# Optimization experiments

Measured on AMD Instinct MI355X. Metric: run time of the kernel, lower is better.

## Reference

```python
import jax, jax.numpy as jnp
import numpy as np

DMODEL = 1024
DK = 64
DHEAD = 16
DEPTH = DK * DHEAD
N, LQ, L = 2, 2048, 2048


def setup_inputs() -> dict:
    key = jax.random.key(0)
    ks = jax.random.split(key, 12)
    s = 1.0 / np.sqrt(DMODEL)
    inp = {
        'x': jax.random.normal(ks[0], (N, LQ, DMODEL), jnp.float32),
        'y': jax.random.normal(ks[1], (N, L, DMODEL), jnp.float32),
        'mask': jnp.tril(jnp.ones((LQ, L), dtype=bool)),  # causal
        'Wq': jax.random.normal(ks[2], (DMODEL, DEPTH), jnp.float32) * s,
        'bq': jnp.zeros((DEPTH,), jnp.float32),
        'Wk': jax.random.normal(ks[3], (DMODEL, DEPTH), jnp.float32) * s,
        'bk': jnp.zeros((DEPTH,), jnp.float32),
        'Wv': jax.random.normal(ks[4], (DMODEL, DEPTH), jnp.float32) * s,
        'bv': jnp.zeros((DEPTH,), jnp.float32),
        'Wo': jax.random.normal(ks[5], (DEPTH, DMODEL), jnp.float32) * (1.0 / np.sqrt(DEPTH)),
        'bo': jnp.zeros((DMODEL,), jnp.float32),
    }
    return inp


def reference(x, y, mask, Wq, bq, Wk, bk, Wv, bv, Wo, bo):
    fac = 1.0 / np.sqrt(DK)
    q = (x @ Wq + bq).reshape(N, LQ, DHEAD, DK).transpose(0, 2, 1, 3)  # N,H,Lq,dk
    k = (y @ Wk + bk).reshape(N, L, DHEAD, DK).transpose(0, 2, 1, 3)   # N,H,L,dk
    v = (y @ Wv + bv).reshape(N, L, DHEAD, DK).transpose(0, 2, 1, 3)   # N,H,L,dk
    scores = jnp.einsum('bhqd,bhkd->bhqk', q, k) * fac                 # N,H,Lq,L
    scores = jnp.where(mask, scores, -1e9)  # mask broadcasts over N,H
    attn = jax.nn.softmax(scores, axis=-1)
    out = jnp.einsum('bhqk,bhkd->bhqd', attn, v)                        # N,H,Lq,dk
    out = out.transpose(0, 2, 1, 3).reshape(N, LQ, DEPTH)
    return out @ Wo + bo
```

## Files before the change

kernel.cpp:

```cpp
#include <hip/hip_runtime.h>
#include <hip/hip_bf16.h>

typedef __attribute__((ext_vector_type(8))) short short8;
typedef __attribute__((ext_vector_type(4))) float floatx4;

#define LQ 2048
#define DM 1024
#define NH 16
#define LOG2E 1.44269504088896f

typedef __attribute__((address_space(1))) void gas_t;
typedef __attribute__((address_space(3))) void las_t;

__device__ __forceinline__ void async16(const __hip_bfloat16* g, __hip_bfloat16* l) {
    __builtin_amdgcn_global_load_lds((gas_t*)g, (las_t*)l, 16, 0, 0);
}

__global__ __launch_bounds__(256) void prep_all(
    const float* __restrict__ x,  const float* __restrict__ y,
    const float* __restrict__ Wq, const float* __restrict__ Wk,
    const float* __restrict__ Wv, const float* __restrict__ Wo,
    __hip_bfloat16* __restrict__ xb,  __hip_bfloat16* __restrict__ yb,
    __hip_bfloat16* __restrict__ Wqt, __hip_bfloat16* __restrict__ Wkt,
    __hip_bfloat16* __restrict__ Wvt, __hip_bfloat16* __restrict__ Wot)
{
    __shared__ float tile[64][65];
    const int t  = threadIdx.x;
    const int bx = blockIdx.x;

    if (bx < 4096) {
        const float* in = (bx < 2048) ? x : y;
        __hip_bfloat16* out = (bx < 2048) ? xb : yb;
        const int i = ((bx & 2047) * 256 + t) * 8;
        float4 a0 = ((const float4*)(in + i))[0];
        float4 a1 = ((const float4*)(in + i))[1];
        union { __hip_bfloat16 h[8]; uint4 u; } pk;
        pk.h[0] = __float2bfloat16(a0.x); pk.h[1] = __float2bfloat16(a0.y);
        pk.h[2] = __float2bfloat16(a0.z); pk.h[3] = __float2bfloat16(a0.w);
        pk.h[4] = __float2bfloat16(a1.x); pk.h[5] = __float2bfloat16(a1.y);
        pk.h[6] = __float2bfloat16(a1.z); pk.h[7] = __float2bfloat16(a1.w);
        *(uint4*)(out + i) = pk.u;
        return;
    }

    const int r    = bx - 4096;
    const int wsel = r >> 8;
    const int tid  = r & 255;
    const int n0   = (tid & 15) * 64, k0 = (tid >> 4) * 64;
    const float* W = (wsel == 0) ? Wq : (wsel == 1) ? Wk : (wsel == 2) ? Wv : Wo;
    __hip_bfloat16* Wt = (wsel == 0) ? Wqt : (wsel == 1) ? Wkt : (wsel == 2) ? Wvt : Wot;

    const int rr0 = t >> 4, c4 = (t & 15) * 4;
#pragma unroll
    for (int rr = 0; rr < 64; rr += 16) {
        float4 v = *(const float4*)&W[(size_t)(k0 + rr0 + rr) * DM + n0 + c4];
        tile[rr0 + rr][c4 + 0] = v.x; tile[rr0 + rr][c4 + 1] = v.y;
        tile[rr0 + rr][c4 + 2] = v.z; tile[rr0 + rr][c4 + 3] = v.w;
    }
    __syncthreads();
    const int nr = t >> 2, kc = (t & 3) * 16;
    union { __hip_bfloat16 h[16]; uint4 u[2]; } pk;
#pragma unroll
    for (int i = 0; i < 16; ++i) pk.h[i] = __float2bfloat16(tile[kc + i][nr]);
    uint4* dst = (uint4*)&Wt[(size_t)(n0 + nr) * DM + k0 + kc];
    dst[0] = pk.u[0];
    dst[1] = pk.u[1];
}

__global__ __launch_bounds__(512) void gemm_qkv(
    const __hip_bfloat16* __restrict__ xb,
    const __hip_bfloat16* __restrict__ yb,
    const __hip_bfloat16* __restrict__ Bt,
    const float* __restrict__ bq, const float* __restrict__ bk,
    const float* __restrict__ bv,
    __hip_bfloat16* __restrict__ Qb, __hip_bfloat16* __restrict__ Kb,
    __hip_bfloat16* __restrict__ Vt,
    float qscl)
{
    constexpr int BM = 256, BN = 256, Kd = 1024;
    constexpr int NHS = Kd / 32;
    __shared__ __align__(16) __hip_bfloat16 As[4][256 * 32];
    __shared__ __align__(16) __hip_bfloat16 Bs[4][256 * 32];

    const int t    = threadIdx.x;
    const int w    = t >> 6;
    const int lane = t & 63;
    const int quad = lane >> 4;
    const int l16  = lane & 15;
    const int wm   = w & 1;
    const int wn   = w >> 1;

    const int f  = blockIdx.x;
    const int rx = f & 7;
    const int rr = f >> 3;
    const int bx = (rx & 1) * 6 + rr % 6;
    const int by = (rx >> 1) * 4 + rr / 6;
    const int m0 = by * BM;
    const int n0 = bx * BN;

    const int region = n0 >> 10;
    const int nl     = n0 & 1023;

    const __hip_bfloat16* A = (region == 0) ? xb : yb;

    floatx4 acc[8][4];
#pragma unroll
    for (int i = 0; i < 8; ++i)
#pragma unroll
        for (int j = 0; j < 4; ++j) acc[i][j] = (floatx4){0.f, 0.f, 0.f, 0.f};

    auto stageA = [&](int h) {
        const int k0 = h * 32, slot = h & 3;
#pragma unroll
        for (int l = 0; l < 2; ++l) {
            const int c   = l * 512 + t;
            const int row = c >> 2;
            const int ch  = (c & 3) ^ ((row >> 1) & 3);
            async16(A + (size_t)(m0 + row) * Kd + k0 + ch * 8, &As[slot][c * 8]);
        }
    };
    auto stageB = [&](int h) {
        const int k0 = h * 32, slot = h & 3;
#pragma unroll
        for (int l = 0; l < 2; ++l) {
            const int c   = l * 512 + t;
            const int row = c >> 2;
            const int ch  = (c & 3) ^ ((row >> 1) & 3);
            async16(Bt + (size_t)(n0 + row) * Kd + k0 + ch * 8, &Bs[slot][c * 8]);
        }
    };

    stageA(0); stageB(0); stageA(1); stageB(1);
    asm volatile("s_waitcnt vmcnt(4)" ::: "memory");
    __builtin_amdgcn_sched_barrier(0);
    __builtin_amdgcn_s_barrier();

    const int csw = (l16 >> 1) & 3;

    for (int h = 0; h < NHS; ++h) {
        const int slot = h & 3;
        const __hip_bfloat16* as = &As[slot][0];
        const __hip_bfloat16* bs = &Bs[slot][0];
        short8 af[8], bf[4];

#pragma unroll
        for (int nj = 0; nj < 4; ++nj) {
            const int row = wn * 64 + nj * 16 + l16;
            bf[nj] = *(const short8*)&bs[row * 32 + (quad ^ csw) * 8];
        }
#pragma unroll
        for (int mi = 0; mi < 4; ++mi) {
            const int row = wm * 128 + mi * 16 + l16;
            af[mi] = *(const short8*)&as[row * 32 + (quad ^ csw) * 8];
        }
        if (h + 2 < NHS) stageA(h + 2);
        __builtin_amdgcn_s_barrier();
        asm volatile("s_waitcnt lgkmcnt(0)" ::: "memory");
        __builtin_amdgcn_sched_barrier(0);
        __builtin_amdgcn_s_setprio(1);
#pragma unroll
        for (int mi = 0; mi < 4; ++mi)
#pragma unroll
            for (int nj = 0; nj < 4; ++nj)
                acc[mi][nj] = __builtin_amdgcn_mfma_f32_16x16x32_bf16(af[mi], bf[nj], acc[mi][nj], 0, 0, 0);
        __builtin_amdgcn_s_setprio(0);
        __builtin_amdgcn_s_barrier();

#pragma unroll
        for (int mi = 4; mi < 8; ++mi) {
            const int row = wm * 128 + mi * 16 + l16;
            af[mi] = *(const short8*)&as[row * 32 + (quad ^ csw) * 8];
        }
        if (h + 2 < NHS) stageB(h + 2);
        __builtin_amdgcn_s_barrier();
        asm volatile("s_waitcnt lgkmcnt(0)" ::: "memory");
        __builtin_amdgcn_sched_barrier(0);
        __builtin_amdgcn_s_setprio(1);
#pragma unroll
        for (int mi = 4; mi < 8; ++mi)
#pragma unroll
            for (int nj = 0; nj < 4; ++nj)
                acc[mi][nj] = __builtin_amdgcn_mfma_f32_16x16x32_bf16(af[mi], bf[nj], acc[mi][nj], 0, 0, 0);
        __builtin_amdgcn_s_setprio(0);
        if (h + 2 < NHS)      asm volatile("s_waitcnt vmcnt(4)" ::: "memory");
        else                  asm volatile("s_waitcnt vmcnt(0)" ::: "memory");
        __builtin_amdgcn_sched_barrier(0);
        __builtin_amdgcn_s_barrier();
    }

    if (region < 2) {
        __hip_bfloat16* C    = (region == 0) ? Qb : Kb;
        const float*    bias = (region == 0) ? bq : bk;
        const float     scl  = (region == 0) ? qscl : 1.0f;
#pragma unroll
        for (int j = 0; j < 4; ++j) {
            const int col = nl + wn * 64 + j * 16 + l16;
            const float bvv = bias[col];
#pragma unroll
            for (int mi = 0; mi < 8; ++mi) {
#pragma unroll
                for (int r = 0; r < 4; ++r) {
                    const int row = m0 + wm * 128 + mi * 16 + quad * 4 + r;
                    C[(size_t)row * 1024 + col] = __float2bfloat16((acc[mi][j][r] + bvv) * scl);
                }
            }
        }
    } else {
#pragma unroll
        for (int j = 0; j < 4; ++j) {
            const int col = nl + wn * 64 + j * 16 + l16;
            const float bvv = bv[col];
#pragma unroll
            for (int mi = 0; mi < 8; ++mi) {
                const int row0 = m0 + wm * 128 + mi * 16 + quad * 4;
                union { __hip_bfloat16 h4[4]; uint2 u; } pk;
#pragma unroll
                for (int r = 0; r < 4; ++r)
                    pk.h4[r] = __float2bfloat16(acc[mi][j][r] + bvv);
                *(uint2*)&Vt[((size_t)((row0 >> 11) * 1024 + col)) * 2048 + (row0 & 2047)] = pk.u;
            }
        }
    }
}

__global__ __launch_bounds__(256) void gemm_o(
    const __hip_bfloat16* __restrict__ A,
    const __hip_bfloat16* __restrict__ Bt,
    const float* __restrict__ bias,
    float* __restrict__ C,
    int M)
{
    constexpr int BM = 64, BN = 128, BK = 32, Kd = 1024, NIT = Kd / BK;
    __shared__ __align__(16) __hip_bfloat16 As[3][BM * BK];
    __shared__ __align__(16) __hip_bfloat16 Bs[3][BN * BK];

    const int t    = threadIdx.x;
    const int w    = t >> 6;
    const int lane = t & 63;
    const int quad = lane >> 4;
    const int l16  = lane & 15;
    const int wm   = w & 1;
    const int wn   = w >> 1;

    const int f  = blockIdx.x;
    const int rx = f & 7;
    const int rr = f >> 3;
    const int bx = (rx & 1) * 4 + (rr & 3);
    const int by = (rx >> 1) * 16 + (rr >> 2);
    const int m0 = by * BM;
    const int n0 = bx * BN;

    const int lrow = lane >> 2;
    const int lcol = (lane & 3) * 8;

    floatx4 acc[2][4];
#pragma unroll
    for (int i = 0; i < 2; ++i)
#pragma unroll
        for (int j = 0; j < 4; ++j) acc[i][j] = (floatx4){0.f, 0.f, 0.f, 0.f};

    auto stage = [&](int k0, int buf) {
#pragma unroll
        for (int s = 0; s < 3; ++s) {
            const int seg = w * 3 + s;
            if (seg < 4) {
                async16(A + (size_t)(m0 + seg * 16 + lrow) * Kd + k0 + lcol,
                        &As[buf][seg * 16 * BK]);
            } else {
                const int bs = seg - 4;
                async16(Bt + (size_t)(n0 + bs * 16 + lrow) * Kd + k0 + lcol,
                        &Bs[buf][bs * 16 * BK]);
            }
        }
    };

    stage(0, 0);
    stage(BK, 1);
    int cur = 0;
    for (int i = 0; i < NIT; ++i) {
        if (i < NIT - 1) asm volatile("s_waitcnt vmcnt(3)" ::: "memory");
        else             asm volatile("s_waitcnt vmcnt(0)" ::: "memory");
        __builtin_amdgcn_sched_barrier(0);
        __builtin_amdgcn_s_barrier();
        if (i + 2 < NIT) stage((i + 2) * BK, (cur + 2 >= 3) ? cur - 1 : cur + 2);

        short8 af[2], bf[4];
#pragma unroll
        for (int ii = 0; ii < 2; ++ii)
            af[ii] = *(const short8*)&As[cur][(wm * 32 + ii * 16 + l16) * BK + quad * 8];
#pragma unroll
        for (int j = 0; j < 4; ++j)
            bf[j] = *(const short8*)&Bs[cur][(wn * 64 + j * 16 + l16) * BK + quad * 8];
#pragma unroll
        for (int ii = 0; ii < 2; ++ii)
#pragma unroll
            for (int j = 0; j < 4; ++j)
                acc[ii][j] = __builtin_amdgcn_mfma_f32_16x16x32_bf16(af[ii], bf[j], acc[ii][j], 0, 0, 0);
        cur = (cur + 1 >= 3) ? 0 : cur + 1;
    }

#pragma unroll
    for (int j = 0; j < 4; ++j) {
        const int col = n0 + wn * 64 + j * 16 + l16;
        const float bvf = bias[col];
#pragma unroll
        for (int i = 0; i < 2; ++i) {
#pragma unroll
            for (int r = 0; r < 4; ++r) {
                const int row = m0 + wm * 32 + i * 16 + quad * 4 + r;
                C[(size_t)row * 1024 + col] = acc[i][j][r] + bvf;
            }
        }
    }
}

template <bool A_IS_F32, bool OUT_F32, bool TRANSV = false>
__global__ __launch_bounds__(256) void gemm64(
    const void* __restrict__ Av,
    const float* __restrict__ B,
    const float* __restrict__ bias,
    void* __restrict__ Cv,
    int M, int N, int K, float scale)
{
    __shared__ __align__(16) __hip_bfloat16 As[64][40];
    __shared__ __align__(16) __hip_bfloat16 Bs[64][40];

    const int t    = threadIdx.x;
    const int wave = t >> 6;
    const int lane = t & 63;
    const int quad = lane >> 4;
    const int l16  = lane & 15;
    const int m0   = blockIdx.y * 64;
    const int n0   = blockIdx.x * 64;

    floatx4 acc[4];
#pragma unroll
    for (int i = 0; i < 4; ++i) acc[i] = (floatx4){0.f, 0.f, 0.f, 0.f};

    const int arow = t >> 2, acol = (t & 3) * 8;
    const int bkk  = t >> 3, bnn  = (t & 7) * 8;

    for (int k0 = 0; k0 < K; k0 += 32) {
        if constexpr (A_IS_F32) {
            const float* A = (const float*)Av;
            const float* ap = A + (size_t)(m0 + arow) * K + k0 + acol;
            float4 a0 = ((const float4*)ap)[0];
            float4 a1 = ((const float4*)ap)[1];
            union { __hip_bfloat16 h[8]; short8 s; } up;
            up.h[0] = __float2bfloat16(a0.x); up.h[1] = __float2bfloat16(a0.y);
            up.h[2] = __float2bfloat16(a0.z); up.h[3] = __float2bfloat16(a0.w);
            up.h[4] = __float2bfloat16(a1.x); up.h[5] = __float2bfloat16(a1.y);
            up.h[6] = __float2bfloat16(a1.z); up.h[7] = __float2bfloat16(a1.w);
            *(short8*)(&As[arow][acol]) = up.s;
        } else {
            const __hip_bfloat16* A = (const __hip_bfloat16*)Av;
            uint4 av = *(const uint4*)(A + (size_t)(m0 + arow) * K + k0 + acol);
            *(uint4*)(&As[arow][acol]) = av;
        }
        {
            const float* bp = B + (size_t)(k0 + bkk) * N + n0 + bnn;
            float4 b0 = ((const float4*)bp)[0];
            float4 b1 = ((const float4*)bp)[1];
            Bs[bnn + 0][bkk] = __float2bfloat16(b0.x);
            Bs[bnn + 1][bkk] = __float2bfloat16(b0.y);
            Bs[bnn + 2][bkk] = __float2bfloat16(b0.z);
            Bs[bnn + 3][bkk] = __float2bfloat16(b0.w);
            Bs[bnn + 4][bkk] = __float2bfloat16(b1.x);
            Bs[bnn + 5][bkk] = __float2bfloat16(b1.y);
            Bs[bnn + 6][bkk] = __float2bfloat16(b1.z);
            Bs[bnn + 7][bkk] = __float2bfloat16(b1.w);
        }
        __syncthreads();

        short8 afrag = *(const short8*)(&As[wave * 16 + l16][quad * 8]);
#pragma unroll
        for (int nt = 0; nt < 4; ++nt) {
            short8 bfrag = *(const short8*)(&Bs[nt * 16 + l16][quad * 8]);
            acc[nt] = __builtin_amdgcn_mfma_f32_16x16x32_bf16(afrag, bfrag, acc[nt], 0, 0, 0);
        }
        __syncthreads();
    }

#pragma unroll
    for (int nt = 0; nt < 4; ++nt) {
        const int col = n0 + nt * 16 + l16;
        const float bvf = bias[col];
        if constexpr (TRANSV) {
            const int row0 = m0 + wave * 16 + quad * 4;
            union { __hip_bfloat16 h4[4]; uint2 u; } pk;
#pragma unroll
            for (int r = 0; r < 4; ++r)
                pk.h4[r] = __float2bfloat16(acc[nt][r] + bvf);
            *(uint2*)&((__hip_bfloat16*)Cv)[((size_t)((row0 >> 11) * 1024 + col)) * 2048 + (row0 & 2047)] = pk.u;
        } else {
#pragma unroll
            for (int r = 0; r < 4; ++r) {
                const int row = m0 + wave * 16 + quad * 4 + r;
                const float v = (acc[nt][r] + bvf) * scale;
                if constexpr (OUT_F32) ((float*)Cv)[(size_t)row * N + col] = v;
                else ((__hip_bfloat16*)Cv)[(size_t)row * N + col] = __float2bfloat16(v);
            }
        }
    }
}

#define PP 72

__global__ __launch_bounds__(256, 2) void attn_mfma10(
    const __hip_bfloat16* __restrict__ Q,
    const __hip_bfloat16* __restrict__ K,
    const __hip_bfloat16* __restrict__ Vt,
    __hip_bfloat16* __restrict__ O)
{
    __shared__ __align__(16) __hip_bfloat16 KtS[3][64 * 64];
    __shared__ __align__(16) __hip_bfloat16 VtS[3][64 * 64];
    __shared__ __align__(16) __hip_bfloat16 PsQ[128 * PP];

    const int t    = threadIdx.x;
    const int w    = t >> 6;
    const int lane = t & 63;
    const int quad = lane >> 4;
    const int l16  = lane & 15;

    const int f   = blockIdx.x;
    const int xcd = f & 7;
    const int u   = f >> 3;
    const int pi  = u >> 4;
    const int qr  = u & 15;
    const int qx  = (pi & 2) ? (15 - qr) : qr;
    const int p   = xcd * 4 + pi;
    const int h   = p & 15;
    const int b   = p >> 4;
    const int q0  = qx * 128;

    const size_t rowbase = (size_t)b * LQ;
    const int    hcol    = h * 64;
    const size_t vbase   = (size_t)(b * NH + h) * 64 * LQ;

    const int r8 = l16 & 7;

    auto stage = [&](int j0n, int buf) {
#pragma unroll
        for (int rnd = 0; rnd < 2; ++rnd) {
            const int c   = rnd * 256 + t;
            const int row = c >> 3;
            const int ch  = (c & 7) ^ (row & 7);
            async16(K + (rowbase + j0n + row) * DM + hcol + ch * 8,
                    &KtS[buf][c * 8]);
            async16(Vt + vbase + (size_t)row * LQ + j0n + ch * 8,
                    &VtS[buf][c * 8]);
        }
    };

    {
        const int qrow = t >> 1, qseg = (t & 1) * 32;
        const uint4* src = (const uint4*)(Q + (rowbase + q0 + qrow) * DM + hcol + qseg);
        uint4* dst = (uint4*)&PsQ[qrow * PP + qseg];
        dst[0] = src[0]; dst[1] = src[1]; dst[2] = src[2]; dst[3] = src[3];
    }
    stage(0, 0);
    stage(64, 1);

    short8 qf[2][2];
#pragma unroll
    for (int g = 0; g < 2; ++g)
#pragma unroll
        for (int hh = 0; hh < 2; ++hh)
            qf[g][hh] = *(const short8*)&PsQ[(w * 32 + g * 16 + l16) * PP + hh * 32 + quad * 8];

    __hip_bfloat16* Pw = &PsQ[(w * 32) * PP];

    float l_i[2] = {0.f, 0.f};
    floatx4 o[2][4];
#pragma unroll
    for (int g = 0; g < 2; ++g)
#pragma unroll
        for (int i = 0; i < 4; ++i) o[g][i] = (floatx4){0.f, 0.f, 0.f, 0.f};

    const int wq_lo  = q0 + w * 32;
    const int wq_hi  = wq_lo + 31;
    const int ntiles = 2 * qx + 2;

    int cur = 0;
    for (int jt = 0; jt < ntiles; ++jt) {
        const int j0 = jt * 64;

        if (jt < ntiles - 1) asm volatile("s_waitcnt vmcnt(4)" ::: "memory");
        else                 asm volatile("s_waitcnt vmcnt(0)" ::: "memory");
        __builtin_amdgcn_sched_barrier(0);
        __builtin_amdgcn_s_barrier();
        if (jt + 2 < ntiles) stage(j0 + 128, (cur + 2 >= 3) ? cur - 1 : cur + 2);

        if (j0 <= wq_hi) {
            const bool bnd = (j0 + 63 > wq_lo);
#pragma unroll
            for (int jc = 0; jc < 4; ++jc) {
                const __hip_bfloat16* kr = &KtS[cur][(jc * 16 + l16) * 64];
                short8 ak0 = *(const short8*)&kr[((quad    ) ^ r8) * 8];
                short8 ak1 = *(const short8*)&kr[((quad + 4) ^ r8) * 8];
#pragma unroll
                for (int g = 0; g < 2; ++g) {
                    floatx4 z = (floatx4){0.f, 0.f, 0.f, 0.f};
                    z = __builtin_amdgcn_mfma_f32_16x16x32_bf16(ak0, qf[g][0], z, 0, 0, 0);
                    z = __builtin_amdgcn_mfma_f32_16x16x32_bf16(ak1, qf[g][1], z, 0, 0, 0);
                    if (bnd) {
                        const int qg = wq_lo + g * 16 + l16;
#pragma unroll
                        for (int r = 0; r < 4; ++r) {
                            const int j = j0 + jc * 16 + quad * 4 + r;
                            if (j > qg) z[r] = -1e30f;
                        }
                    }
                    union { __hip_bfloat16 h4[4]; uint2 u; } pk;
#pragma unroll
                    for (int r = 0; r < 4; ++r) {
                        const float e = __builtin_amdgcn_exp2f(z[r]);
                        l_i[g] += e;
                        pk.h4[r] = __float2bfloat16(e);
                    }
                    *(uint2*)&Pw[(g * 16 + l16) * PP + jc * 16 + quad * 4] = pk.u;
                }
            }
            short8 pa[2][2];
#pragma unroll
            for (int g = 0; g < 2; ++g) {
                pa[g][0] = *(const short8*)&Pw[(g * 16 + l16) * PP + quad * 8];
                pa[g][1] = *(const short8*)&Pw[(g * 16 + l16) * PP + 32 + quad * 8];
            }
            __builtin_amdgcn_s_setprio(1);
#pragma unroll
            for (int subf = 0; subf < 4; ++subf) {
                const __hip_bfloat16* vr = &VtS[cur][(subf * 16 + l16) * 64];
                short8 vb0 = *(const short8*)&vr[((quad    ) ^ r8) * 8];
                short8 vb1 = *(const short8*)&vr[((quad + 4) ^ r8) * 8];
#pragma unroll
                for (int g = 0; g < 2; ++g) {
                    o[g][subf] = __builtin_amdgcn_mfma_f32_16x16x32_bf16(pa[g][0], vb0, o[g][subf], 0, 0, 0);
                    o[g][subf] = __builtin_amdgcn_mfma_f32_16x16x32_bf16(pa[g][1], vb1, o[g][subf], 0, 0, 0);
                }
            }
            __builtin_amdgcn_s_setprio(0);
        }
        cur = (cur + 1 >= 3) ? 0 : cur + 1;
    }

#pragma unroll
    for (int g = 0; g < 2; ++g) {
        l_i[g] += __shfl_xor(l_i[g], 16);
        l_i[g] += __shfl_xor(l_i[g], 32);
#pragma unroll
        for (int r = 0; r < 4; ++r) {
            const float linv = 1.0f / __shfl(l_i[g], quad * 4 + r);
            const size_t row = rowbase + q0 + w * 32 + g * 16 + quad * 4 + r;
#pragma unroll
            for (int subf = 0; subf < 4; ++subf)
                O[row * DM + hcol + subf * 16 + l16] = __float2bfloat16(o[g][subf][r] * linv);
        }
    }
}

extern "C" void kernel_launch(void* const* d_in, const int* in_sizes, int n_in,
                              void* d_out, int out_size, void* d_ws, size_t ws_size,
                              hipStream_t stream)
{
    (void)in_sizes; (void)n_in; (void)out_size;

    const float* x  = (const float*)d_in[0];
    const float* y  = (const float*)d_in[1];
    const float* Wq = (const float*)d_in[3];
    const float* bq = (const float*)d_in[4];
    const float* Wk = (const float*)d_in[5];
    const float* bk = (const float*)d_in[6];
    const float* Wv = (const float*)d_in[7];
    const float* bv = (const float*)d_in[8];
    const float* Wo = (const float*)d_in[9];
    const float* bo = (const float*)d_in[10];

    const size_t NTOK = (size_t)2 * LQ * DM;
    const size_t MM   = (size_t)DM * DM;
    const int    M    = 2 * LQ;
    const float  QSCL = 0.125f * LOG2E;

    __hip_bfloat16* Qb  = (__hip_bfloat16*)d_ws;
    __hip_bfloat16* Kb  = Qb + NTOK;
    __hip_bfloat16* Vtb = Kb + NTOK;
    __hip_bfloat16* Ab  = Vtb + NTOK;

    const size_t need = (4 * NTOK + 2 * NTOK + 4 * MM) * sizeof(__hip_bfloat16);
    const dim3 agrid(512, 1, 1);

    if (ws_size >= need) {
        __hip_bfloat16* xb  = Ab + NTOK;
        __hip_bfloat16* yb  = xb + NTOK;
        __hip_bfloat16* Wqt = yb + NTOK;
        __hip_bfloat16* Wkt = Wqt + MM;
        __hip_bfloat16* Wvt = Wkt + MM;
        __hip_bfloat16* Wot = Wvt + MM;
        (void)Wkt; (void)Wvt;

        prep_all<<<5120, 256, 0, stream>>>(x, y, Wq, Wk, Wv, Wo,
                                           xb, yb, Wqt, Wkt, Wvt, Wot);

        gemm_qkv<<<192, 512, 0, stream>>>(xb, yb, Wqt, bq, bk, bv, Qb, Kb, Vtb, QSCL);
        attn_mfma10<<<agrid, 256, 0, stream>>>(Qb, Kb, Vtb, Ab);
        gemm_o<<<512, 256, 0, stream>>>(Ab, Wot, bo, (float*)d_out, M);
    } else {
        const dim3 gblk(DM / 64, M / 64);
        gemm64<true,  false><<<gblk, 256, 0, stream>>>(x, Wq, bq, Qb, M, DM, DM, QSCL);
        gemm64<true,  false><<<gblk, 256, 0, stream>>>(y, Wk, bk, Kb, M, DM, DM, 1.0f);
        gemm64<true,  false, true><<<gblk, 256, 0, stream>>>(y, Wv, bv, Vtb, M, DM, DM, 1.0f);
        attn_mfma10<<<agrid, 256, 0, stream>>>(Qb, Kb, Vtb, Ab);
        gemm64<false, true ><<<gblk, 256, 0, stream>>>(Ab, Wo, bo, (float*)d_out, M, DM, DM, 1.0f);
    }
}
```

Baseline: 216.8 us.

## Software-pipeline attention PV product one tile behind QK scores

Restructures the attention loop so that the P·V MFMA for the previous tile runs at the start of the next iteration, after K fragments for the current tile are loaded. The V staging ring grows from three to four buffers so the previous tile's V survives the extra iteration. The aim is to overlap the P write/read latency through LDS and the exp work with MFMA issue. In exchange it uses more LDS (an extra 8KB) and holds more live registers for the prefetched K fragments, which could reduce occupancy.

```diff
diff --git a/kernel.cpp b/kernel.cpp
--- a/kernel.cpp
+++ b/kernel.cpp
@@ -406,14 +406,14 @@
 
 #define PP 72
 
-__global__ __launch_bounds__(256, 2) void attn_mfma10(
+__global__ __launch_bounds__(256, 2) void attn_mfma11(
     const __hip_bfloat16* __restrict__ Q,
     const __hip_bfloat16* __restrict__ K,
     const __hip_bfloat16* __restrict__ Vt,
     __hip_bfloat16* __restrict__ O)
 {
     __shared__ __align__(16) __hip_bfloat16 KtS[3][64 * 64];
-    __shared__ __align__(16) __hip_bfloat16 VtS[3][64 * 64];
+    __shared__ __align__(16) __hip_bfloat16 VtS[4][64 * 64];
     __shared__ __align__(16) __hip_bfloat16 PsQ[128 * PP];
 
     const int t    = threadIdx.x;
@@ -439,16 +439,18 @@
 
     const int r8 = l16 & 7;
 
-    auto stage = [&](int j0n, int buf) {
+    auto stage = [&](int j0n, int jtile) {
+        const int ks = jtile % 3;
+        const int vs = jtile & 3;
 #pragma unroll
         for (int rnd = 0; rnd < 2; ++rnd) {
             const int c   = rnd * 256 + t;
             const int row = c >> 3;
             const int ch  = (c & 7) ^ (row & 7);
             async16(K + (rowbase + j0n + row) * DM + hcol + ch * 8,
-                    &KtS[buf][c * 8]);
+                    &KtS[ks][c * 8]);
             async16(Vt + vbase + (size_t)row * LQ + j0n + ch * 8,
-                    &VtS[buf][c * 8]);
+                    &VtS[vs][c * 8]);
         }
     };
 
@@ -481,7 +483,9 @@
     const int wq_hi  = wq_lo + 31;
     const int ntiles = 2 * qx + 2;
 
-    int cur = 0;
+    short8 pa[2][2];
+    int    pslot = -1;
+
     for (int jt = 0; jt < ntiles; ++jt) {
         const int j0 = jt * 64;
 
@@ -489,20 +493,47 @@
         else                 asm volatile("s_waitcnt vmcnt(0)" ::: "memory");
         __builtin_amdgcn_sched_barrier(0);
         __builtin_amdgcn_s_barrier();
-        if (jt + 2 < ntiles) stage(j0 + 128, (cur + 2 >= 3) ? cur - 1 : cur + 2);
-
-        if (j0 <= wq_hi) {
+        if (jt + 2 < ntiles) stage(j0 + 128, jt + 2);
+
+        const bool active = (j0 <= wq_hi);
+
+        short8 ak[4][2];
+        if (active) {
+#pragma unroll
+            for (int jc = 0; jc < 4; ++jc) {
+                const __hip_bfloat16* kr = &KtS[jt % 3][(jc * 16 + l16) * 64];
+                ak[jc][0] = *(const short8*)&kr[((quad    ) ^ r8) * 8];
+                ak[jc][1] = *(const short8*)&kr[((quad + 4) ^ r8) * 8];
+            }
+        }
+
+        if (pslot >= 0) {
+            __builtin_amdgcn_s_setprio(1);
+#pragma unroll
+            for (int subf = 0; subf < 4; ++subf) {
+                const __hip_bfloat16* vr = &VtS[pslot][(subf * 16 + l16) * 64];
+                short8 vb0 = *(const short8*)&vr[((quad    ) ^ r8) * 8];
+                short8 vb1 = *(const short8*)&vr[((quad + 4) ^ r8) * 8];
+#pragma unroll
+                for (int g = 0; g < 2; ++g) {
+                    o[g][subf] = __builtin_amdgcn_mfma_f32_16x16x32_bf16(pa[g][0], vb0, o[g][subf], 0, 0, 0);
+                    o[g][subf] = __builtin_amdgcn_mfma_f32_16x16x32_bf16(pa[g][1], vb1, o[g][subf], 0, 0, 0);
+                }
+            }
+            __builtin_amdgcn_s_setprio(0);
+            pslot = -1;
+        }
+
+        if (active) {
             const bool bnd = (j0 + 63 > wq_lo);
+            __builtin_amdgcn_s_setprio(1);
 #pragma unroll
             for (int jc = 0; jc < 4; ++jc) {
-                const __hip_bfloat16* kr = &KtS[cur][(jc * 16 + l16) * 64];
-                short8 ak0 = *(const short8*)&kr[((quad    ) ^ r8) * 8];
-                short8 ak1 = *(const short8*)&kr[((quad + 4) ^ r8) * 8];
 #pragma unroll
                 for (int g = 0; g < 2; ++g) {
                     floatx4 z = (floatx4){0.f, 0.f, 0.f, 0.f};
-                    z = __builtin_amdgcn_mfma_f32_16x16x32_bf16(ak0, qf[g][0], z, 0, 0, 0);
-                    z = __builtin_amdgcn_mfma_f32_16x16x32_bf16(ak1, qf[g][1], z, 0, 0, 0);
+                    z = __builtin_amdgcn_mfma_f32_16x16x32_bf16(ak[jc][0], qf[g][0], z, 0, 0, 0);
+                    z = __builtin_amdgcn_mfma_f32_16x16x32_bf16(ak[jc][1], qf[g][1], z, 0, 0, 0);
                     if (bnd) {
                         const int qg = wq_lo + g * 16 + l16;
 #pragma unroll
@@ -521,27 +552,28 @@
                     *(uint2*)&Pw[(g * 16 + l16) * PP + jc * 16 + quad * 4] = pk.u;
                 }
             }
-            short8 pa[2][2];
+            __builtin_amdgcn_s_setprio(0);
 #pragma unroll
             for (int g = 0; g < 2; ++g) {
                 pa[g][0] = *(const short8*)&Pw[(g * 16 + l16) * PP + quad * 8];
                 pa[g][1] = *(const short8*)&Pw[(g * 16 + l16) * PP + 32 + quad * 8];
             }
-            __builtin_amdgcn_s_setprio(1);
-#pragma unroll
-            for (int subf = 0; subf < 4; ++subf) {
-                const __hip_bfloat16* vr = &VtS[cur][(subf * 16 + l16) * 64];
-                short8 vb0 = *(const short8*)&vr[((quad    ) ^ r8) * 8];
-                short8 vb1 = *(const short8*)&vr[((quad + 4) ^ r8) * 8];
-#pragma unroll
-                for (int g = 0; g < 2; ++g) {
-                    o[g][subf] = __builtin_amdgcn_mfma_f32_16x16x32_bf16(pa[g][0], vb0, o[g][subf], 0, 0, 0);
-                    o[g][subf] = __builtin_amdgcn_mfma_f32_16x16x32_bf16(pa[g][1], vb1, o[g][subf], 0, 0, 0);
-                }
-            }
-            __builtin_amdgcn_s_setprio(0);
-        }
-        cur = (cur + 1 >= 3) ? 0 : cur + 1;
+            pslot = jt & 3;
+        }
+    }
+
+    if (pslot >= 0) {
+#pragma unroll
+        for (int subf = 0; subf < 4; ++subf) {
+            const __hip_bfloat16* vr = &VtS[pslot][(subf * 16 + l16) * 64];
+            short8 vb0 = *(const short8*)&vr[((quad    ) ^ r8) * 8];
+            short8 vb1 = *(const short8*)&vr[((quad + 4) ^ r8) * 8];
+#pragma unroll
+            for (int g = 0; g < 2; ++g) {
+                o[g][subf] = __builtin_amdgcn_mfma_f32_16x16x32_bf16(pa[g][0], vb0, o[g][subf], 0, 0, 0);
+                o[g][subf] = __builtin_amdgcn_mfma_f32_16x16x32_bf16(pa[g][1], vb1, o[g][subf], 0, 0, 0);
+            }
+        }
     }
 
 #pragma unroll
@@ -602,14 +634,14 @@
                                            xb, yb, Wqt, Wkt, Wvt, Wot);
 
         gemm_qkv<<<192, 512, 0, stream>>>(xb, yb, Wqt, bq, bk, bv, Qb, Kb, Vtb, QSCL);
-        attn_mfma10<<<agrid, 256, 0, stream>>>(Qb, Kb, Vtb, Ab);
+        attn_mfma11<<<agrid, 256, 0, stream>>>(Qb, Kb, Vtb, Ab);
         gemm_o<<<512, 256, 0, stream>>>(Ab, Wot, bo, (float*)d_out, M);
     } else {
         const dim3 gblk(DM / 64, M / 64);
         gemm64<true,  false><<<gblk, 256, 0, stream>>>(x, Wq, bq, Qb, M, DM, DM, QSCL);
         gemm64<true,  false><<<gblk, 256, 0, stream>>>(y, Wk, bk, Kb, M, DM, DM, 1.0f);
         gemm64<true,  false, true><<<gblk, 256, 0, stream>>>(y, Wv, bv, Vtb, M, DM, DM, 1.0f);
-        attn_mfma10<<<agrid, 256, 0, stream>>>(Qb, Kb, Vtb, Ab);
+        attn_mfma11<<<agrid, 256, 0, stream>>>(Qb, Kb, Vtb, Ab);
         gemm64<false, true ><<<gblk, 256, 0, stream>>>(Ab, Wo, bo, (float*)d_out, M, DM, DM, 1.0f);
     }
 }
```

Result: no change. 213.4 us (-1.6%).
